# Performance work log

Hardware: AMD Instinct MI355X
Metric: run time of the kernel (lower is better)

Reference implementation:

```python
import jax, jax.numpy as jnp
import numpy as np
from jax import lax

EPS = 1e-5
B, C, H, W = 64, 32, 128, 128

def _bn(x, gamma, beta, mean, var):
    # inference-mode batchnorm over channel dim (NCHW)
    scale = gamma / jnp.sqrt(var + EPS)
    return x * scale[None, :, None, None] + (beta - mean * scale)[None, :, None, None]

def _conv3x3(x, w, b):
    # 3x3 conv, stride 1, padding 1, NCHW / OIHW
    y = lax.conv_general_dilated(x, w, window_strides=(1, 1), padding=((1, 1), (1, 1)),
                                 dimension_numbers=('NCHW', 'OIHW', 'NCHW'))
    return y + b[None, :, None, None]


def setup_inputs() -> dict:
    key = jax.random.key(0)
    ks = jax.random.split(key, 13)
    fan_in = C * 9
    return {
        'x': jax.random.normal(ks[0], (B, C, H, W), jnp.float32),
        'bn1_gamma': jax.random.uniform(ks[1], (C,), jnp.float32, 0.5, 1.5),
        'bn1_beta': jax.random.normal(ks[2], (C,), jnp.float32) * 0.1,
        'bn1_mean': jax.random.normal(ks[3], (C,), jnp.float32) * 0.1,
        'bn1_var': jax.random.uniform(ks[4], (C,), jnp.float32, 0.5, 1.5),
        'w1': jax.random.normal(ks[5], (C, C, 3, 3), jnp.float32) / np.sqrt(fan_in),
        'b1': jax.random.normal(ks[6], (C,), jnp.float32) * 0.01,
        'bn2_gamma': jax.random.uniform(ks[7], (C,), jnp.float32, 0.5, 1.5),
        'bn2_beta': jax.random.normal(ks[8], (C,), jnp.float32) * 0.1,
        'bn2_mean': jax.random.normal(ks[9], (C,), jnp.float32) * 0.1,
        'bn2_var': jax.random.uniform(ks[10], (C,), jnp.float32, 0.5, 1.5),
        'w2': jax.random.normal(ks[11], (C, C, 3, 3), jnp.float32) / np.sqrt(fan_in),
        'b2': jax.random.normal(ks[12], (C,), jnp.float32) * 0.01,
    }


def reference(x, bn1_gamma, bn1_beta, bn1_mean, bn1_var, w1, b1,
              bn2_gamma, bn2_beta, bn2_mean, bn2_var, w2, b2):
    # BN -> ReLU -> conv3x3 -> (dropout: identity in eval) -> BN -> ReLU -> conv3x3
    h = jnp.maximum(_bn(x, bn1_gamma, bn1_beta, bn1_mean, bn1_var), 0.0)
    h = _conv3x3(h, w1, b1)
    h = jnp.maximum(_bn(h, bn2_gamma, bn2_beta, bn2_mean, bn2_var), 0.0)
    h = _conv3x3(h, w2, b2)
    # stride=1 and in_channels==channels -> identity shortcut
    return h + x
```

## Files before the change

### kernel.cpp

```cpp
#include <hip/hip_runtime.h>

#define EPSV 1e-5f

typedef __bf16 bf16x8 __attribute__((ext_vector_type(8)));
typedef float f32x4 __attribute__((ext_vector_type(4)));
typedef unsigned short ushort8 __attribute__((ext_vector_type(8)));

__device__ __forceinline__ void gload16(const void* g, void* l) {
  __builtin_amdgcn_global_load_lds(
      (const __attribute__((address_space(1))) unsigned int*)g,
      (__attribute__((address_space(3))) unsigned int*)l, 16, 0, 0);
}

__global__ __launch_bounds__(256) void prep_weights(
    const float* __restrict__ w1, const float* __restrict__ b1,
    const float* __restrict__ g2, const float* __restrict__ be2,
    const float* __restrict__ m2, const float* __restrict__ v2,
    const float* __restrict__ w2,
    __bf16* __restrict__ wf1, __bf16* __restrict__ wf2,
    float* __restrict__ bias1p) {
  int i = blockIdx.x * 256 + threadIdx.x;
  int conv = i / 9216;
  int rem  = i % 9216;
  int tap  = rem >> 10;
  int r2   = rem & 1023;
  int half = r2 >> 9;
  int lane = (r2 >> 3) & 63;
  int j    = r2 & 7;
  int ci = ((lane >> 4) << 3) + j;
  int co = half * 16 + (lane & 15);
  float val = (conv ? w2 : w1)[(co * 32 + ci) * 9 + tap];
  if (!conv) val *= g2[co] * rsqrtf(v2[co] + EPSV);
  (conv ? wf2 : wf1)[rem] = (__bf16)val;
  if (blockIdx.x == 0 && threadIdx.x < 32) {
    int c = threadIdx.x;
    float s2 = g2[c] * rsqrtf(v2[c] + EPSV);
    bias1p[c] = s2 * b1[c] + (be2[c] - m2[c] * s2);
  }
}

__global__ __launch_bounds__(256) void bn_relu_pack(
    const float* __restrict__ x,
    const float* __restrict__ g1, const float* __restrict__ be1,
    const float* __restrict__ m1, const float* __restrict__ v1,
    unsigned short* __restrict__ xb) {
  __shared__ __align__(16) unsigned short sh[128 * 40];
  int t = threadIdx.x;
  int b = blockIdx.x >> 7, h = blockIdx.x & 127;
  int c = t >> 3, w0 = (t & 7) * 16;
  float sc = g1[c] * rsqrtf(v1[c] + EPSV);
  float sf = be1[c] - m1[c] * sc;
  const float* src = x + (((long)(b * 32 + c) * 128 + h) * 128 + w0);
  #pragma unroll
  for (int k = 0; k < 16; k += 4) {
    f32x4 v = *reinterpret_cast<const f32x4*>(src + k);
    #pragma unroll
    for (int q = 0; q < 4; q++) {
      float val = fmaxf(v[q] * sc + sf, 0.0f);
      sh[(w0 + k + q) * 40 + c] = __builtin_bit_cast(unsigned short, (__bf16)val);
    }
  }
  __syncthreads();
  int pix = t >> 1, hh = t & 1;
  int q2 = (pix >> 1) & 3;
  unsigned short* dst = xb + (long)blockIdx.x * (128 * 32);
  #pragma unroll
  for (int cc = 0; cc < 2; cc++) {
    int cb = 2 * hh + cc;
    int s = cb ^ q2;
    ushort8 vv = *reinterpret_cast<const ushort8*>(&sh[pix * 40 + cb * 8]);
    *reinterpret_cast<ushort8*>(dst + (pix * 4 + s) * 8) = vv;
  }
}

template <int PASS>
__global__ __launch_bounds__(256, PASS == 1 ? 2 : 3) void conv3x3(
    const unsigned short* __restrict__ in,
    const __bf16* __restrict__ wfrag,
    const float* __restrict__ bias,
    const float* __restrict__ xres,
    unsigned short* __restrict__ outb,
    float* __restrict__ outf) {
  __shared__ __align__(16) unsigned short tile[6 * 4160];
  int t = threadIdx.x;
  int lane = t & 63, wv = t >> 6;
  int b = blockIdx.x >> 5;
  int h0 = (blockIdx.x & 31) * 4;

  bf16x8 Bf[9][2];
  #pragma unroll
  for (int tap = 0; tap < 9; tap++)
    #pragma unroll
    for (int hf = 0; hf < 2; hf++)
      Bf[tap][hf] = reinterpret_cast<const bf16x8*>(wfrag)[(tap * 2 + hf) * 64 + lane];
  float bco[2] = { bias[lane & 15], bias[16 + (lane & 15)] };

  int cb = lane >> 4;
  int offs[2][3];
  #pragma unroll
  for (int g = 0; g < 2; g++)
    #pragma unroll
    for (int dx = 0; dx < 3; dx++) {
      int w = wv * 32 + g * 16 + (lane & 15) + dx - 1;
      int s = cb ^ ((w >> 1) & 3);
      offs[g][dx] = (w + 1) * 64 + s * 16;
    }

  #pragma unroll
  for (int rr = 0; rr < 6; rr++) {
    int hr = h0 - 1 + rr;
    unsigned short* base = &tile[rr * 4160];
    if (hr < 0 || hr >= 128) {
      ushort8 z{};
      for (int k = t; k < 520; k += 256)
        *reinterpret_cast<ushort8*>(base + k * 8) = z;
    } else {
      const char* src = reinterpret_cast<const char*>(in) +
                        ((long)(b * 128 + hr) * 128) * 64;
      #pragma unroll
      for (int i = 0; i < 2; i++) {
        int kb = (wv * 2 + i) * 64;
        gload16(src + (long)(kb + lane) * 16,
                reinterpret_cast<char*>(base) + 64 + kb * 16);
      }
    }
  }
  if (t < 48) {
    int sl = t >> 3, r2 = t & 7;
    int phys = (r2 >> 2) * 129, ch = r2 & 3;
    *reinterpret_cast<ushort8*>(&tile[sl * 4160 + phys * 32 + ch * 8]) = ushort8{};
  }
  __syncthreads();

  f32x4 acc4[4][2][2] = {};
  #pragma unroll
  for (int r = 0; r < 4; r++) {
    #pragma unroll
    for (int dy = 0; dy < 3; dy++) {
      const char* rowbase = reinterpret_cast<const char*>(&tile[(r + dy) * 4160]);
      #pragma unroll
      for (int dx = 0; dx < 3; dx++) {
        #pragma unroll
        for (int g = 0; g < 2; g++) {
          bf16x8 a = *reinterpret_cast<const bf16x8*>(rowbase + offs[g][dx]);
          acc4[r][g][0] = __builtin_amdgcn_mfma_f32_16x16x32_bf16(a, Bf[dy * 3 + dx][0], acc4[r][g][0], 0, 0, 0);
          acc4[r][g][1] = __builtin_amdgcn_mfma_f32_16x16x32_bf16(a, Bf[dy * 3 + dx][1], acc4[r][g][1], 0, 0, 0);
        }
      }
    }
    if (PASS == 2) {
      int hr = h0 + r;
      #pragma unroll
      for (int g = 0; g < 2; g++)
        #pragma unroll
        for (int hf = 0; hf < 2; hf++) {
          int co = hf * 16 + (lane & 15);
          int pix0 = wv * 32 + g * 16 + ((lane >> 4) << 2);
          long idx = ((long)(b * 32 + co) * 128 + hr) * 128 + pix0;
          f32x4 xr = *reinterpret_cast<const f32x4*>(xres + idx);
          f32x4 o;
          #pragma unroll
          for (int j = 0; j < 4; j++) o[j] = acc4[r][g][hf][j] + bco[hf] + xr[j];
          *reinterpret_cast<f32x4*>(outf + idx) = o;
        }
    }
  }

  if (PASS == 1) {
    __syncthreads();
    #pragma unroll
    for (int r = 0; r < 4; r++)
      #pragma unroll
      for (int g = 0; g < 2; g++)
        #pragma unroll
        for (int hf = 0; hf < 2; hf++) {
          int co = hf * 16 + (lane & 15);
          #pragma unroll
          for (int j = 0; j < 4; j++) {
            int pix = wv * 32 + g * 16 + ((lane >> 4) << 2) + j;
            float val = fmaxf(acc4[r][g][hf][j] + bco[hf], 0.0f);
            int byte = r * 8192 + pix * 64 + (((co >> 3) ^ ((pix >> 1) & 3)) << 4) + (co & 7) * 2;
            *reinterpret_cast<unsigned short*>(reinterpret_cast<char*>(tile) + byte) =
                __builtin_bit_cast(unsigned short, (__bf16)val);
          }
        }
    __syncthreads();
    unsigned short* dst = outb + ((long)(b * 128 + h0) * 128) * 32;
    #pragma unroll
    for (int i = 0; i < 8; i++) {
      int u = i * 256 + t;
      *reinterpret_cast<ushort8*>(dst + u * 8) =
          *reinterpret_cast<const ushort8*>(reinterpret_cast<const char*>(tile) + u * 16);
    }
  }
}

extern "C" void kernel_launch(void* const* d_in, const int* in_sizes, int n_in,
                              void* d_out, int out_size, void* d_ws, size_t ws_size,
                              hipStream_t stream) {
  const float* x   = (const float*)d_in[0];
  const float* g1  = (const float*)d_in[1];
  const float* be1 = (const float*)d_in[2];
  const float* m1  = (const float*)d_in[3];
  const float* v1  = (const float*)d_in[4];
  const float* w1  = (const float*)d_in[5];
  const float* b1  = (const float*)d_in[6];
  const float* g2  = (const float*)d_in[7];
  const float* be2 = (const float*)d_in[8];
  const float* m2  = (const float*)d_in[9];
  const float* v2  = (const float*)d_in[10];
  const float* w2  = (const float*)d_in[11];
  const float* b2  = (const float*)d_in[12];

  char* ws = (char*)d_ws;
  unsigned short* xb = (unsigned short*)ws;
  unsigned short* hb = (unsigned short*)(ws + 67108864);
  __bf16* wf1   = (__bf16*)(ws + 134217728);
  __bf16* wf2   = (__bf16*)(ws + 134217728 + 18432);
  float*  bias1p = (float*)(ws + 134217728 + 36864);

  prep_weights<<<dim3(72), dim3(256), 0, stream>>>(w1, b1, g2, be2, m2, v2, w2, wf1, wf2, bias1p);
  bn_relu_pack<<<dim3(8192), dim3(256), 0, stream>>>(x, g1, be1, m1, v1, xb);
  conv3x3<1><<<dim3(2048), dim3(256), 0, stream>>>(xb, wf1, bias1p, nullptr, hb, nullptr);
  conv3x3<2><<<dim3(2048), dim3(256), 0, stream>>>(hb, wf2, b2, x, nullptr, (float*)d_out);
}
```

Measured before the change: 362.3 us.

## Fuse BN1+ReLU into conv1 tile load and read conv2 inputs directly from global

Removes the separate bn_relu_pack kernel and its bf16 intermediate buffer: conv1 now reads fp32 x directly, applies BN1+ReLU in registers and writes the swizzled bf16 tile to LDS. This saves a full write and read of the packed activation. Conv2 drops the LDS tile and loads A fragments straight from global/L2, with clamping and masking at the borders. Both kernels remap block indices so consecutive blocks spread across XCDs. The risk is redundant halo reads of fp32 x and uncached repeated global loads in conv2.

Result: faster. 326.7 us (-9.8%).

```diff
diff --git a/kernel.cpp b/kernel.cpp
--- a/kernel.cpp
+++ b/kernel.cpp
@@ -4,21 +4,18 @@
 
 typedef __bf16 bf16x8 __attribute__((ext_vector_type(8)));
 typedef float f32x4 __attribute__((ext_vector_type(4)));
+typedef float f32x2 __attribute__((ext_vector_type(2)));
 typedef unsigned short ushort8 __attribute__((ext_vector_type(8)));
-
-__device__ __forceinline__ void gload16(const void* g, void* l) {
-  __builtin_amdgcn_global_load_lds(
-      (const __attribute__((address_space(1))) unsigned int*)g,
-      (__attribute__((address_space(3))) unsigned int*)l, 16, 0, 0);
-}
 
 __global__ __launch_bounds__(256) void prep_weights(
     const float* __restrict__ w1, const float* __restrict__ b1,
     const float* __restrict__ g2, const float* __restrict__ be2,
     const float* __restrict__ m2, const float* __restrict__ v2,
     const float* __restrict__ w2,
+    const float* __restrict__ g1, const float* __restrict__ be1,
+    const float* __restrict__ m1, const float* __restrict__ v1,
     __bf16* __restrict__ wf1, __bf16* __restrict__ wf2,
-    float* __restrict__ bias1p) {
+    float* __restrict__ bias1p, float* __restrict__ sc1, float* __restrict__ sf1) {
   int i = blockIdx.x * 256 + threadIdx.x;
   int conv = i / 9216;
   int rem  = i % 9216;
@@ -37,55 +34,59 @@
     float s2 = g2[c] * rsqrtf(v2[c] + EPSV);
     bias1p[c] = s2 * b1[c] + (be2[c] - m2[c] * s2);
   }
-}
-
-__global__ __launch_bounds__(256) void bn_relu_pack(
+  if (blockIdx.x == 0 && threadIdx.x >= 64 && threadIdx.x < 96) {
+    int c = threadIdx.x - 64;
+    float s = g1[c] * rsqrtf(v1[c] + EPSV);
+    sc1[c] = s;
+    sf1[c] = be1[c] - m1[c] * s;
+  }
+}
+
+__global__ __launch_bounds__(256, 2) void bnconv1(
     const float* __restrict__ x,
-    const float* __restrict__ g1, const float* __restrict__ be1,
-    const float* __restrict__ m1, const float* __restrict__ v1,
-    unsigned short* __restrict__ xb) {
-  __shared__ __align__(16) unsigned short sh[128 * 40];
-  int t = threadIdx.x;
-  int b = blockIdx.x >> 7, h = blockIdx.x & 127;
-  int c = t >> 3, w0 = (t & 7) * 16;
-  float sc = g1[c] * rsqrtf(v1[c] + EPSV);
-  float sf = be1[c] - m1[c] * sc;
-  const float* src = x + (((long)(b * 32 + c) * 128 + h) * 128 + w0);
-  #pragma unroll
-  for (int k = 0; k < 16; k += 4) {
-    f32x4 v = *reinterpret_cast<const f32x4*>(src + k);
-    #pragma unroll
-    for (int q = 0; q < 4; q++) {
-      float val = fmaxf(v[q] * sc + sf, 0.0f);
-      sh[(w0 + k + q) * 40 + c] = __builtin_bit_cast(unsigned short, (__bf16)val);
-    }
-  }
-  __syncthreads();
-  int pix = t >> 1, hh = t & 1;
-  int q2 = (pix >> 1) & 3;
-  unsigned short* dst = xb + (long)blockIdx.x * (128 * 32);
-  #pragma unroll
-  for (int cc = 0; cc < 2; cc++) {
-    int cb = 2 * hh + cc;
-    int s = cb ^ q2;
-    ushort8 vv = *reinterpret_cast<const ushort8*>(&sh[pix * 40 + cb * 8]);
-    *reinterpret_cast<ushort8*>(dst + (pix * 4 + s) * 8) = vv;
-  }
-}
-
-template <int PASS>
-__global__ __launch_bounds__(256, PASS == 1 ? 2 : 3) void conv3x3(
-    const unsigned short* __restrict__ in,
-    const __bf16* __restrict__ wfrag,
-    const float* __restrict__ bias,
-    const float* __restrict__ xres,
-    unsigned short* __restrict__ outb,
-    float* __restrict__ outf) {
+    const float* __restrict__ sc1, const float* __restrict__ sf1,
+    const __bf16* __restrict__ wfrag, const float* __restrict__ bias,
+    unsigned short* __restrict__ outb) {
   __shared__ __align__(16) unsigned short tile[6 * 4160];
-  int t = threadIdx.x;
-  int lane = t & 63, wv = t >> 6;
-  int b = blockIdx.x >> 5;
-  int h0 = (blockIdx.x & 31) * 4;
+  char* tb = reinterpret_cast<char*>(tile);
+  int t = threadIdx.x, lane = t & 63, wv = t >> 6;
+  int Bw = blockIdx.x;
+  int logical = (Bw & 7) * 256 + (Bw >> 3);
+  int b = logical >> 5, h0 = (logical & 31) * 4;
+
+  float sc[8], sf[8];
+  #pragma unroll
+  for (int cc = 0; cc < 8; cc++) { sc[cc] = sc1[wv * 8 + cc]; sf[cc] = sf1[wv * 8 + cc]; }
+
+  int wbyte0 = (2 * lane + 1) * 64 + ((wv ^ (lane & 3)) << 4);
+  #pragma unroll
+  for (int k = 0; k < 6; k++) {
+    int hr = h0 - 1 + k;
+    char* dst = tb + k * 8320 + wbyte0;
+    if (hr >= 0 && hr < 128) {
+      const float* src = x + (long)(b * 32 + wv * 8) * 16384 + hr * 128 + 2 * lane;
+      float p0[8], p1[8];
+      #pragma unroll
+      for (int cc = 0; cc < 8; cc++) {
+        f32x2 v = *reinterpret_cast<const f32x2*>(src + cc * 16384);
+        p0[cc] = fmaxf(fmaf(v[0], sc[cc], sf[cc]), 0.0f);
+        p1[cc] = fmaxf(fmaf(v[1], sc[cc], sf[cc]), 0.0f);
+      }
+      bf16x8 a0, a1;
+      #pragma unroll
+      for (int cc = 0; cc < 8; cc++) { a0[cc] = (__bf16)p0[cc]; a1[cc] = (__bf16)p1[cc]; }
+      *reinterpret_cast<bf16x8*>(dst) = a0;
+      *reinterpret_cast<bf16x8*>(dst + 64) = a1;
+    } else {
+      *reinterpret_cast<bf16x8*>(dst) = bf16x8{};
+      *reinterpret_cast<bf16x8*>(dst + 64) = bf16x8{};
+    }
+  }
+  if (t < 48) {
+    int sl = t >> 3, r2 = t & 7;
+    int phys = (r2 >> 2) * 129, ch = r2 & 3;
+    *reinterpret_cast<ushort8*>(&tile[sl * 4160 + phys * 32 + ch * 8]) = ushort8{};
+  }
 
   bf16x8 Bf[9][2];
   #pragma unroll
@@ -106,92 +107,117 @@
       offs[g][dx] = (w + 1) * 64 + s * 16;
     }
 
-  #pragma unroll
-  for (int rr = 0; rr < 6; rr++) {
-    int hr = h0 - 1 + rr;
-    unsigned short* base = &tile[rr * 4160];
-    if (hr < 0 || hr >= 128) {
-      ushort8 z{};
-      for (int k = t; k < 520; k += 256)
-        *reinterpret_cast<ushort8*>(base + k * 8) = z;
-    } else {
-      const char* src = reinterpret_cast<const char*>(in) +
-                        ((long)(b * 128 + hr) * 128) * 64;
-      #pragma unroll
-      for (int i = 0; i < 2; i++) {
-        int kb = (wv * 2 + i) * 64;
-        gload16(src + (long)(kb + lane) * 16,
-                reinterpret_cast<char*>(base) + 64 + kb * 16);
-      }
-    }
-  }
-  if (t < 48) {
-    int sl = t >> 3, r2 = t & 7;
-    int phys = (r2 >> 2) * 129, ch = r2 & 3;
-    *reinterpret_cast<ushort8*>(&tile[sl * 4160 + phys * 32 + ch * 8]) = ushort8{};
-  }
   __syncthreads();
 
   f32x4 acc4[4][2][2] = {};
   #pragma unroll
-  for (int r = 0; r < 4; r++) {
+  for (int r = 0; r < 4; r++)
     #pragma unroll
     for (int dy = 0; dy < 3; dy++) {
-      const char* rowbase = reinterpret_cast<const char*>(&tile[(r + dy) * 4160]);
-      #pragma unroll
-      for (int dx = 0; dx < 3; dx++) {
+      const char* rowbase = tb + (r + dy) * 8320;
+      #pragma unroll
+      for (int dx = 0; dx < 3; dx++)
         #pragma unroll
         for (int g = 0; g < 2; g++) {
           bf16x8 a = *reinterpret_cast<const bf16x8*>(rowbase + offs[g][dx]);
           acc4[r][g][0] = __builtin_amdgcn_mfma_f32_16x16x32_bf16(a, Bf[dy * 3 + dx][0], acc4[r][g][0], 0, 0, 0);
           acc4[r][g][1] = __builtin_amdgcn_mfma_f32_16x16x32_bf16(a, Bf[dy * 3 + dx][1], acc4[r][g][1], 0, 0, 0);
         }
-      }
-    }
-    if (PASS == 2) {
-      int hr = h0 + r;
-      #pragma unroll
-      for (int g = 0; g < 2; g++)
-        #pragma unroll
-        for (int hf = 0; hf < 2; hf++) {
-          int co = hf * 16 + (lane & 15);
-          int pix0 = wv * 32 + g * 16 + ((lane >> 4) << 2);
-          long idx = ((long)(b * 32 + co) * 128 + hr) * 128 + pix0;
-          f32x4 xr = *reinterpret_cast<const f32x4*>(xres + idx);
-          f32x4 o;
+    }
+
+  __syncthreads();
+  #pragma unroll
+  for (int r = 0; r < 4; r++)
+    #pragma unroll
+    for (int g = 0; g < 2; g++)
+      #pragma unroll
+      for (int hf = 0; hf < 2; hf++) {
+        int co = hf * 16 + (lane & 15);
+        #pragma unroll
+        for (int j = 0; j < 4; j++) {
+          int pix = wv * 32 + g * 16 + ((lane >> 4) << 2) + j;
+          float val = fmaxf(acc4[r][g][hf][j] + bco[hf], 0.0f);
+          int byte = r * 8192 + pix * 64 + (((co >> 3) ^ ((pix >> 1) & 3)) << 4) + (co & 7) * 2;
+          *reinterpret_cast<unsigned short*>(tb + byte) =
+              __builtin_bit_cast(unsigned short, (__bf16)val);
+        }
+      }
+  __syncthreads();
+  unsigned short* dst = outb + ((long)(b * 128 + h0) * 128) * 32;
+  #pragma unroll
+  for (int i = 0; i < 8; i++) {
+    int u = i * 256 + t;
+    *reinterpret_cast<ushort8*>(dst + u * 8) =
+        *reinterpret_cast<const ushort8*>(tb + u * 16);
+  }
+}
+
+__global__ __launch_bounds__(256, 2) void conv2_direct(
+    const unsigned short* __restrict__ hb,
+    const __bf16* __restrict__ wfrag, const float* __restrict__ bias,
+    const float* __restrict__ xres, float* __restrict__ outf) {
+  int t = threadIdx.x, lane = t & 63, wv = t >> 6;
+  int Bw = blockIdx.x;
+  int logical = (Bw & 7) * 256 + (Bw >> 3);
+  int b = logical >> 5, h0 = (logical & 31) * 4;
+
+  bf16x8 Bf[9][2];
+  #pragma unroll
+  for (int tap = 0; tap < 9; tap++)
+    #pragma unroll
+    for (int hf = 0; hf < 2; hf++)
+      Bf[tap][hf] = reinterpret_cast<const bf16x8*>(wfrag)[(tap * 2 + hf) * 64 + lane];
+  float bco[2] = { bias[lane & 15], bias[16 + (lane & 15)] };
+
+  int cb = lane >> 4;
+  int coloff[2][3];
+  bool colbad[2][3];
+  #pragma unroll
+  for (int g = 0; g < 2; g++)
+    #pragma unroll
+    for (int dx = 0; dx < 3; dx++) {
+      int w = wv * 32 + g * 16 + (lane & 15) + dx - 1;
+      colbad[g][dx] = (w < 0) || (w > 127);
+      int wc = w < 0 ? 0 : (w > 127 ? 127 : w);
+      int s = cb ^ ((wc >> 1) & 3);
+      coloff[g][dx] = wc * 64 + s * 16;
+    }
+
+  const char* hbase = reinterpret_cast<const char*>(hb) + (long)b * 128 * 8192;
+
+  #pragma unroll
+  for (int r = 0; r < 4; r++) {
+    f32x4 acc[2][2] = {};
+    #pragma unroll
+    for (int dy = 0; dy < 3; dy++) {
+      int hr_in = h0 + r + dy - 1;
+      if (hr_in >= 0 && hr_in < 128) {
+        const char* rowb = hbase + (long)hr_in * 8192;
+        #pragma unroll
+        for (int dx = 0; dx < 3; dx++)
           #pragma unroll
-          for (int j = 0; j < 4; j++) o[j] = acc4[r][g][hf][j] + bco[hf] + xr[j];
-          *reinterpret_cast<f32x4*>(outf + idx) = o;
-        }
-    }
-  }
-
-  if (PASS == 1) {
-    __syncthreads();
-    #pragma unroll
-    for (int r = 0; r < 4; r++)
-      #pragma unroll
-      for (int g = 0; g < 2; g++)
-        #pragma unroll
-        for (int hf = 0; hf < 2; hf++) {
-          int co = hf * 16 + (lane & 15);
-          #pragma unroll
-          for (int j = 0; j < 4; j++) {
-            int pix = wv * 32 + g * 16 + ((lane >> 4) << 2) + j;
-            float val = fmaxf(acc4[r][g][hf][j] + bco[hf], 0.0f);
-            int byte = r * 8192 + pix * 64 + (((co >> 3) ^ ((pix >> 1) & 3)) << 4) + (co & 7) * 2;
-            *reinterpret_cast<unsigned short*>(reinterpret_cast<char*>(tile) + byte) =
-                __builtin_bit_cast(unsigned short, (__bf16)val);
+          for (int g = 0; g < 2; g++) {
+            bf16x8 a = *reinterpret_cast<const bf16x8*>(rowb + coloff[g][dx]);
+            if (colbad[g][dx]) a = bf16x8{};
+            acc[g][0] = __builtin_amdgcn_mfma_f32_16x16x32_bf16(a, Bf[dy * 3 + dx][0], acc[g][0], 0, 0, 0);
+            acc[g][1] = __builtin_amdgcn_mfma_f32_16x16x32_bf16(a, Bf[dy * 3 + dx][1], acc[g][1], 0, 0, 0);
           }
-        }
-    __syncthreads();
-    unsigned short* dst = outb + ((long)(b * 128 + h0) * 128) * 32;
-    #pragma unroll
-    for (int i = 0; i < 8; i++) {
-      int u = i * 256 + t;
-      *reinterpret_cast<ushort8*>(dst + u * 8) =
-          *reinterpret_cast<const ushort8*>(reinterpret_cast<const char*>(tile) + u * 16);
-    }
+      }
+    }
+    int hr = h0 + r;
+    #pragma unroll
+    for (int g = 0; g < 2; g++)
+      #pragma unroll
+      for (int hf = 0; hf < 2; hf++) {
+        int co = hf * 16 + (lane & 15);
+        int pix0 = wv * 32 + g * 16 + ((lane >> 4) << 2);
+        long idx = ((long)(b * 32 + co) * 128 + hr) * 128 + pix0;
+        f32x4 xr = *reinterpret_cast<const f32x4*>(xres + idx);
+        f32x4 o;
+        #pragma unroll
+        for (int j = 0; j < 4; j++) o[j] = acc[g][hf][j] + bco[hf] + xr[j];
+        *reinterpret_cast<f32x4*>(outf + idx) = o;
+      }
   }
 }
 
@@ -213,14 +239,15 @@
   const float* b2  = (const float*)d_in[12];
 
   char* ws = (char*)d_ws;
-  unsigned short* xb = (unsigned short*)ws;
-  unsigned short* hb = (unsigned short*)(ws + 67108864);
-  __bf16* wf1   = (__bf16*)(ws + 134217728);
-  __bf16* wf2   = (__bf16*)(ws + 134217728 + 18432);
-  float*  bias1p = (float*)(ws + 134217728 + 36864);
-
-  prep_weights<<<dim3(72), dim3(256), 0, stream>>>(w1, b1, g2, be2, m2, v2, w2, wf1, wf2, bias1p);
-  bn_relu_pack<<<dim3(8192), dim3(256), 0, stream>>>(x, g1, be1, m1, v1, xb);
-  conv3x3<1><<<dim3(2048), dim3(256), 0, stream>>>(xb, wf1, bias1p, nullptr, hb, nullptr);
-  conv3x3<2><<<dim3(2048), dim3(256), 0, stream>>>(hb, wf2, b2, x, nullptr, (float*)d_out);
-}
+  unsigned short* hb = (unsigned short*)ws;
+  __bf16* wf1    = (__bf16*)(ws + 67108864);
+  __bf16* wf2    = (__bf16*)(ws + 67108864 + 18432);
+  float*  bias1p = (float*)(ws + 67108864 + 36864);
+  float*  sc1    = (float*)(ws + 67108864 + 36992);
+  float*  sf1    = (float*)(ws + 67108864 + 37120);
+
+  prep_weights<<<dim3(72), dim3(256), 0, stream>>>(
+      w1, b1, g2, be2, m2, v2, w2, g1, be1, m1, v1, wf1, wf2, bias1p, sc1, sf1);
+  bnconv1<<<dim3(2048), dim3(256), 0, stream>>>(x, sc1, sf1, wf1, bias1p, hb);
+  conv2_direct<<<dim3(2048), dim3(256), 0, stream>>>(hb, wf2, b2, x, (float*)d_out);
+}
```
